# Optimization experiments

Hardware: AMD Instinct MI355X
Metric: run time of the kernel (lower is better)

The kernel has to match this reference:

```python
import jax, jax.numpy as jnp
import numpy as np

EPS = 1e-12  # F.normalize eps

def _l2norm(t):
    n = jnp.linalg.norm(t, axis=-1, keepdims=True)
    return t / jnp.maximum(n, EPS)

def setup_inputs() -> dict:
    key = jax.random.key(0)
    ks = jax.random.split(key, 6)
    B, S, H, M = 4, 4096, 1024, 256
    x = jax.random.normal(ks[0], (B, S, H), dtype=jnp.float32)
    W_query = jax.random.normal(ks[1], (M, H), dtype=jnp.float32) * 0.02
    W_key = jax.random.normal(ks[2], (M, H), dtype=jnp.float32) * 0.02
    W_value = jax.random.normal(ks[3], (M, H), dtype=jnp.float32) * 0.02
    W_out = jax.random.normal(ks[4], (H, M), dtype=jnp.float32) * 0.02
    M0 = jnp.zeros((M, M), dtype=jnp.float32)
    return {"x": x, "W_query": W_query, "W_key": W_key, "W_value": W_value,
            "W_out": W_out, "M0": M0, "chunk_size": 64}

def reference(x, W_query, W_key, W_value, W_out, M0, chunk_size):
    B, S, H = x.shape
    Mdim = W_query.shape[0]
    decay, max_m_norm = 0.99, 10.0
    q = jnp.einsum('bsh,mh->bsm', x, W_query)
    k = _l2norm(jnp.einsum('bsh,mh->bsm', x, W_key))
    v = _l2norm(jnp.einsum('bsh,mh->bsm', x, W_value))
    n_chunks = S // chunk_size
    c = chunk_size
    # (n_chunks, B, c, Mdim) so scan iterates over chunks
    qc = q.reshape(B, n_chunks, c, Mdim).transpose(1, 0, 2, 3)
    kc = k.reshape(B, n_chunks, c, Mdim).transpose(1, 0, 2, 3)
    vc = v.reshape(B, n_chunks, c, Mdim).transpose(1, 0, 2, 3)

    def step(Mst, qkv):
        qch, kch, vch = qkv
        # read with state at start of chunk: q @ M.T
        r = jnp.einsum('bcm,nm->bcn', qch, Mst)
        # uniform write, token-level aggregation
        outer = jnp.einsum('bci,bcj->ij', vch, kch) / (B * c)
        Mn = decay * Mst + outer
        nrm = jnp.linalg.norm(Mn)
        Mn = Mn * (max_m_norm / jnp.maximum(nrm, max_m_norm))
        return Mn, r

    _, r_all = jax.lax.scan(step, M0, (qc, kc, vc))  # (n_chunks, B, c, Mdim)
    retrieved = r_all.transpose(1, 0, 2, 3).reshape(B, S, Mdim)
    out = jnp.einsum('bsm,hm->bsh', retrieved, W_out)
    return out
```

## Files before the change

kernel.cpp:

```cpp
#include <hip/hip_runtime.h>
#include <hip/hip_bf16.h>


typedef __attribute__((ext_vector_type(4))) float  f4;
typedef __attribute__((ext_vector_type(8))) short  bf16x8;

constexpr int   Hdim  = 1024;
constexpr int   Md    = 256;
constexpr int   Ttok  = 16384;
constexpr float DECAY = 0.99f;
constexpr float MAXN  = 10.0f;

__device__ __forceinline__ unsigned short f2bf(float f) {
  union { float f; unsigned u; } v; v.f = f;
  unsigned r = v.u + 0x7FFFu + ((v.u >> 16) & 1u);
  return (unsigned short)(r >> 16);
}
__device__ __forceinline__ float bf2f(unsigned short h) {
  union { unsigned u; float f; } v; v.u = ((unsigned)h) << 16; return v.f;
}
__device__ __forceinline__ unsigned pk2bf(float a, float b) {
  __hip_bfloat162 h = __float22bfloat162_rn(make_float2(a, b));
  unsigned u; __builtin_memcpy(&u, &h, 4); return u;
}

__global__ __launch_bounds__(256) void k1_proj(
    const float* __restrict__ x, const float* __restrict__ Wq,
    const float* __restrict__ Wk, const float* __restrict__ Wv,
    unsigned short* __restrict__ qp, unsigned short* __restrict__ kb,
    unsigned short* __restrict__ vb)
{
  __shared__ unsigned short Als[128][40];
  __shared__ unsigned short Bls[128][40];
  const int tid  = threadIdx.x;
  const int g    = blockIdx.x;
  const int xcd  = g & 7, wq_ = g >> 3;
  const int ntile = wq_ % 6;
  const int strip = xcd * 16 + wq_ / 6;
  const int row0 = strip * 128;
  const int n0   = ntile * 128;
  const int seg  = n0 >> 8;
  const int nw0  = n0 & 255;
  const float* Wseg = (seg == 0) ? Wq : ((seg == 1) ? Wk : Wv);
  unsigned short* dst = (seg == 0) ? qp : ((seg == 1) ? kb : vb);

  const int tk = tid & 7, tr = tid >> 3;
  const int lane = tid & 63, wid = tid >> 6;
  const int wm = wid & 1, wn = wid >> 1;
  const int lr = lane & 15, lq = lane >> 4;

  f4 acc[4][4];
#pragma unroll
  for (int i = 0; i < 4; ++i)
#pragma unroll
    for (int j = 0; j < 4; ++j) acc[i][j] = f4{0.f, 0.f, 0.f, 0.f};

  for (int kk = 0; kk < Hdim; kk += 32) {
#pragma unroll
    for (int p = 0; p < 4; ++p) {
      int row = tr + 32 * p;
      float4 av = *(const float4*)&x[(long)(row0 + row) * Hdim + kk + tk * 4];
      *(uint2*)&Als[row][tk * 4] = make_uint2(pk2bf(av.x, av.y), pk2bf(av.z, av.w));
      float4 bv = *(const float4*)&Wseg[(long)(nw0 + row) * Hdim + kk + tk * 4];
      *(uint2*)&Bls[row][tk * 4] = make_uint2(pk2bf(bv.x, bv.y), pk2bf(bv.z, bv.w));
    }
    __syncthreads();
    bf16x8 af[4], bfr[4];
#pragma unroll
    for (int i = 0; i < 4; ++i) af[i]  = *(const bf16x8*)&Als[wm * 64 + i * 16 + lr][lq * 8];
#pragma unroll
    for (int j = 0; j < 4; ++j) bfr[j] = *(const bf16x8*)&Bls[wn * 64 + j * 16 + lr][lq * 8];
#pragma unroll
    for (int i = 0; i < 4; ++i)
#pragma unroll
      for (int j = 0; j < 4; ++j)
        acc[i][j] = __builtin_amdgcn_mfma_f32_16x16x32_bf16(af[i], bfr[j], acc[i][j], 0, 0, 0);
    __syncthreads();
  }
#pragma unroll
  for (int i = 0; i < 4; ++i)
#pragma unroll
    for (int rr = 0; rr < 4; ++rr) {
      int token = row0 + wm * 64 + i * 16 + lq * 4 + rr;
      int b = token >> 12, s = token & 4095;
      int pidx = (s >> 6) * 256 + b * 64 + (s & 63);
#pragma unroll
      for (int j = 0; j < 4; ++j) {
        int nn = nw0 + wn * 64 + j * 16 + lr;
        dst[pidx * Md + nn] = f2bf(acc[i][j][rr]);
      }
    }
}

__global__ __launch_bounds__(256) void k2_norms(
    const unsigned short* __restrict__ kb, const unsigned short* __restrict__ vb,
    float* __restrict__ innk, float* __restrict__ innv, float* __restrict__ D)
{
  const int tid = threadIdx.x;
  if (blockIdx.x == 0)
    for (int i = tid; i < 4096; i += 256) D[i] = 0.f;
  const int wid = tid >> 6, lane = tid & 63;
  const int row = blockIdx.x * 4 + wid;
  const unsigned short* p = (row < Ttok) ? (kb + (long)row * Md) : (vb + (long)(row - Ttok) * Md);
  ushort4 v = *(const ushort4*)&p[lane * 4];
  float f0 = bf2f(v.x), f1 = bf2f(v.y), f2 = bf2f(v.z), f3 = bf2f(v.w);
  float s = f0 * f0 + f1 * f1 + f2 * f2 + f3 * f3;
#pragma unroll
  for (int off = 32; off; off >>= 1) s += __shfl_xor(s, off);
  if (lane == 0) {
    float inv = 1.0f / fmaxf(sqrtf(s), 1e-12f);
    if (row < Ttok) innk[row] = inv; else innv[row - Ttok] = inv;
  }
}

__global__ __launch_bounds__(256) void k3_outer(
    const unsigned short* __restrict__ kb, const unsigned short* __restrict__ vb,
    const float* __restrict__ innk, const float* __restrict__ innv,
    float* __restrict__ O)
{
  __shared__ unsigned short Als[64][40];
  __shared__ unsigned short Bls[256][40];
  const int tid = threadIdx.x;
  const int t  = blockIdx.y;
  const int i0 = blockIdx.x * 64;
  const int lane = tid & 63, wid = tid >> 6;
  const int lr = lane & 15, lq = lane >> 4;

  f4 acc[16];
#pragma unroll
  for (int q = 0; q < 16; ++q) acc[q] = f4{0.f, 0.f, 0.f, 0.f};

  for (int tok0 = 0; tok0 < 256; tok0 += 32) {
    {
      int il = tid & 63, tl0 = tid >> 6;
#pragma unroll
      for (int p = 0; p < 8; ++p) {
        int tl = tl0 + 4 * p;
        int pidx = t * 256 + tok0 + tl;
        float sc = innv[pidx];
        Als[il][tl] = f2bf(bf2f(vb[(long)pidx * Md + i0 + il]) * sc);
      }
    }
    {
      int j4 = (tid & 63) * 4, tl0 = tid >> 6;
#pragma unroll
      for (int p = 0; p < 8; ++p) {
        int tl = tl0 + 4 * p;
        int pidx = t * 256 + tok0 + tl;
        float sc = innk[pidx];
        ushort4 kv = *(const ushort4*)&kb[(long)pidx * Md + j4];
        Bls[j4 + 0][tl] = f2bf(bf2f(kv.x) * sc);
        Bls[j4 + 1][tl] = f2bf(bf2f(kv.y) * sc);
        Bls[j4 + 2][tl] = f2bf(bf2f(kv.z) * sc);
        Bls[j4 + 3][tl] = f2bf(bf2f(kv.w) * sc);
      }
    }
    __syncthreads();
    bf16x8 af = *(const bf16x8*)&Als[wid * 16 + lr][lq * 8];
#pragma unroll
    for (int j = 0; j < 16; ++j) {
      bf16x8 bfr = *(const bf16x8*)&Bls[j * 16 + lr][lq * 8];
      acc[j] = __builtin_amdgcn_mfma_f32_16x16x32_bf16(af, bfr, acc[j], 0, 0, 0);
    }
    __syncthreads();
  }
  float* Ot = O + (long)t * 65536;
#pragma unroll
  for (int j = 0; j < 16; ++j)
#pragma unroll
    for (int rr = 0; rr < 4; ++rr) {
      int i = i0 + wid * 16 + lq * 4 + rr;
      Ot[i * 256 + j * 16 + lr] = acc[j][rr] * (1.0f / 256.0f);
    }
}

__global__ __launch_bounds__(256) void k4_gram(const float* __restrict__ O, float* __restrict__ D)
{
  __shared__ unsigned short Tls[64][40];
  const int tid = threadIdx.x;
  const int kbase = blockIdx.x * 256;
  const int lane = tid & 63, wid = tid >> 6;
  const int lr = lane & 15, lq = lane >> 4;
  f4 acc[4];
#pragma unroll
  for (int q = 0; q < 4; ++q) acc[q] = f4{0.f, 0.f, 0.f, 0.f};

  for (int kk = 0; kk < 256; kk += 32) {
    int tk = tid & 7, tr = tid >> 3;
#pragma unroll
    for (int p = 0; p < 2; ++p) {
      int row = tr + 32 * p;
      float4 v = *(const float4*)&O[(long)row * 65536 + kbase + kk + tk * 4];
      *(uint2*)&Tls[row][tk * 4] = make_uint2(pk2bf(v.x, v.y), pk2bf(v.z, v.w));
    }
    __syncthreads();
    bf16x8 af = *(const bf16x8*)&Tls[wid * 16 + lr][lq * 8];
#pragma unroll
    for (int nt = 0; nt < 4; ++nt) {
      bf16x8 bfr = *(const bf16x8*)&Tls[nt * 16 + lr][lq * 8];
      acc[nt] = __builtin_amdgcn_mfma_f32_16x16x32_bf16(af, bfr, acc[nt], 0, 0, 0);
    }
    __syncthreads();
  }
#pragma unroll
  for (int nt = 0; nt < 4; ++nt)
#pragma unroll
    for (int rr = 0; rr < 4; ++rr)
      atomicAdd(&D[(wid * 16 + lq * 4 + rr) * 64 + nt * 16 + lr], acc[nt][rr]);
}

__global__ __launch_bounds__(256) void k56_mstate(const float* __restrict__ O,
    const float* __restrict__ D, unsigned short* __restrict__ Mb)
{
  __shared__ float Dl[64 * 65];
  __shared__ float sarr[64];
  const int tid = threadIdx.x;
  const int col = blockIdx.x * 256 + tid;
  float ov[64];
#pragma unroll
  for (int j = 0; j < 64; ++j) ov[j] = O[(long)j * 65536 + col];
  for (int i = tid; i < 4096; i += 256) Dl[(i >> 6) * 65 + (i & 63)] = D[i];
  __syncthreads();
  if (tid < 64) {
    const int lane = tid;
    float w = 0.f, nm2 = 0.f;
    for (int t = 0; t < 64; ++t) {
      float wt   = __shfl(w, t);
      float Dtt  = Dl[t * 65 + t];
      float nmn2 = DECAY * DECAY * nm2 + 2.f * DECAY * wt + Dtt;
      float nrm  = sqrtf(fmaxf(nmn2, 0.f));
      float s    = MAXN / fmaxf(nrm, MAXN);
      if (lane == 0) sarr[t] = s;
      w   = s * (DECAY * w + Dl[t * 65 + lane]);
      nm2 = s * s * nmn2;
    }
  }
  __syncthreads();
  float m = 0.f;
#pragma unroll
  for (int t = 0; t < 64; ++t) {
    Mb[(long)t * 65536 + col] = f2bf(m);
    m = sarr[t] * (DECAY * m + ov[t]);
  }
}

__global__ __launch_bounds__(256) void k7_rgemm(
    const unsigned short* __restrict__ qp, const unsigned short* __restrict__ Mb,
    unsigned short* __restrict__ rb)
{
  __shared__ unsigned short Als[128][40];
  __shared__ unsigned short Bls[128][40];
  const int tid = threadIdx.x;
  const int t = blockIdx.z;
  const int row0 = t * 256 + blockIdx.y * 128;
  const int n0 = blockIdx.x * 128;
  const int lane = tid & 63, wid = tid >> 6;
  const int wm = wid & 1, wn = wid >> 1;
  const int lr = lane & 15, lq = lane >> 4;

  f4 acc[4][4];
#pragma unroll
  for (int i = 0; i < 4; ++i)
#pragma unroll
    for (int j = 0; j < 4; ++j) acc[i][j] = f4{0.f, 0.f, 0.f, 0.f};

  for (int kk = 0; kk < 256; kk += 32) {
    int kcol = (tid & 3) * 8, row = tid >> 2;
#pragma unroll
    for (int p = 0; p < 2; ++p) {
      *(bf16x8*)&Als[row + 64 * p][kcol] =
          *(const bf16x8*)&qp[(long)(row0 + row + 64 * p) * Md + kk + kcol];
      *(bf16x8*)&Bls[row + 64 * p][kcol] =
          *(const bf16x8*)&Mb[(long)t * 65536 + (n0 + row + 64 * p) * Md + kk + kcol];
    }
    __syncthreads();
    bf16x8 af[4], bfr[4];
#pragma unroll
    for (int i = 0; i < 4; ++i) af[i]  = *(const bf16x8*)&Als[wm * 64 + i * 16 + lr][lq * 8];
#pragma unroll
    for (int j = 0; j < 4; ++j) bfr[j] = *(const bf16x8*)&Bls[wn * 64 + j * 16 + lr][lq * 8];
#pragma unroll
    for (int i = 0; i < 4; ++i)
#pragma unroll
      for (int j = 0; j < 4; ++j)
        acc[i][j] = __builtin_amdgcn_mfma_f32_16x16x32_bf16(af[i], bfr[j], acc[i][j], 0, 0, 0);
    __syncthreads();
  }
#pragma unroll
  for (int i = 0; i < 4; ++i)
#pragma unroll
    for (int rr = 0; rr < 4; ++rr) {
      int prow = row0 + wm * 64 + i * 16 + lq * 4 + rr;
#pragma unroll
      for (int j = 0; j < 4; ++j) {
        int n = n0 + wn * 64 + j * 16 + lr;
        rb[(long)prow * Md + n] = f2bf(acc[i][j][rr]);
      }
    }
}

__global__ __launch_bounds__(256) void k8_out(
    const unsigned short* __restrict__ rb, const float* __restrict__ Wo,
    float* __restrict__ out)
{
  __shared__ unsigned short Als[128][40];
  __shared__ unsigned short Bls[128][40];
  const int tid = threadIdx.x;
  const int g = blockIdx.x;
  const int xcd = g & 7, wq_ = g >> 3;
  const int ntile = wq_ & 7;
  const int strip = xcd * 16 + (wq_ >> 3);
  const int n0 = ntile * 128;
  const int row0 = strip * 128;
  const int lane = tid & 63, wid = tid >> 6;
  const int wm = wid & 1, wn = wid >> 1;
  const int lr = lane & 15, lq = lane >> 4;

  f4 acc[4][4];
#pragma unroll
  for (int i = 0; i < 4; ++i)
#pragma unroll
    for (int j = 0; j < 4; ++j) acc[i][j] = f4{0.f, 0.f, 0.f, 0.f};

  for (int kk = 0; kk < 256; kk += 32) {
    {
      int kcol = (tid & 3) * 8, row = tid >> 2;
#pragma unroll
      for (int p = 0; p < 2; ++p)
        *(bf16x8*)&Als[row + 64 * p][kcol] =
            *(const bf16x8*)&rb[(long)(row0 + row + 64 * p) * Md + kk + kcol];
    }
    {
      int tk = tid & 7, tr = tid >> 3;
#pragma unroll
      for (int p = 0; p < 4; ++p) {
        int row = tr + 32 * p;
        float4 v = *(const float4*)&Wo[(long)(n0 + row) * Md + kk + tk * 4];
        *(uint2*)&Bls[row][tk * 4] = make_uint2(pk2bf(v.x, v.y), pk2bf(v.z, v.w));
      }
    }
    __syncthreads();
    bf16x8 af[4], bfr[4];
#pragma unroll
    for (int i = 0; i < 4; ++i) af[i]  = *(const bf16x8*)&Als[wm * 64 + i * 16 + lr][lq * 8];
#pragma unroll
    for (int j = 0; j < 4; ++j) bfr[j] = *(const bf16x8*)&Bls[wn * 64 + j * 16 + lr][lq * 8];
#pragma unroll
    for (int i = 0; i < 4; ++i)
#pragma unroll
      for (int j = 0; j < 4; ++j)
        acc[i][j] = __builtin_amdgcn_mfma_f32_16x16x32_bf16(af[i], bfr[j], acc[i][j], 0, 0, 0);
    __syncthreads();
  }
#pragma unroll
  for (int i = 0; i < 4; ++i)
#pragma unroll
    for (int rr = 0; rr < 4; ++rr) {
      int pidx = row0 + wm * 64 + i * 16 + lq * 4 + rr;
      int t = pidx >> 8, rm = pidx & 255;
      int token = (rm >> 6) * 4096 + t * 64 + (rm & 63);
#pragma unroll
      for (int j = 0; j < 4; ++j) {
        int h = n0 + wn * 64 + j * 16 + lr;
        out[(long)token * Hdim + h] = acc[i][j][rr];
      }
    }
}

extern "C" void kernel_launch(void* const* d_in, const int* in_sizes, int n_in,
                              void* d_out, int out_size, void* d_ws, size_t ws_size,
                              hipStream_t stream) {
  (void)in_sizes; (void)n_in; (void)out_size; (void)ws_size;
  const float* x  = (const float*)d_in[0];
  const float* Wq = (const float*)d_in[1];
  const float* Wk = (const float*)d_in[2];
  const float* Wv = (const float*)d_in[3];
  const float* Wo = (const float*)d_in[4];
  float* out = (float*)d_out;
  char* ws = (char*)d_ws;

  unsigned short* qp = (unsigned short*)(ws + 0);
  unsigned short* kb = (unsigned short*)(ws + 8388608);
  unsigned short* vb = (unsigned short*)(ws + 16777216);
  float* O    = (float*)(ws + 25165824);
  float* D    = (float*)(ws + 41943040);
  float* innk = (float*)(ws + 41959424);
  float* innv = (float*)(ws + 42024960);
  unsigned short* Mb = vb;
  unsigned short* rb = kb;

  k1_proj  <<<768,            256, 0, stream>>>(x, Wq, Wk, Wv, qp, kb, vb);
  k2_norms <<<8192,           256, 0, stream>>>(kb, vb, innk, innv, D);
  k3_outer <<<dim3(4, 64),    256, 0, stream>>>(kb, vb, innk, innv, O);
  k4_gram  <<<256,            256, 0, stream>>>(O, D);
  k56_mstate<<<256,           256, 0, stream>>>(O, D, Mb);
  k7_rgemm <<<dim3(2, 2, 64), 256, 0, stream>>>(qp, Mb, rb);
  k8_out   <<<1024,           256, 0, stream>>>(rb, Wo, out);
}
```

Before: 257.0 us.

## Pre-convert weights to bf16 and stage GEMM tiles via direct global-to-LDS loads

Adds a small kernel that converts Wq/Wk/Wv/Wo to bf16 once per call, so the projection and output GEMMs read half-size weights with no per-tile conversion. The three GEMM kernels now use global_load_lds 16-byte direct copies into XOR-swizzled LDS tiles with a K step of 64. k1 keeps x in fp32 in LDS and converts it to bf16 while building MFMA fragments. k3 also vectorizes its V loads. This trades an extra launch and larger LDS tiles (fp32 A tile in k1) for fewer register round-trips, fewer bank conflicts and fewer barriers per K.

```diff
diff --git a/kernel.cpp b/kernel.cpp
--- a/kernel.cpp
+++ b/kernel.cpp
@@ -23,31 +23,52 @@
   __hip_bfloat162 h = __float22bfloat162_rn(make_float2(a, b));
   unsigned u; __builtin_memcpy(&u, &h, 4); return u;
 }
+__device__ __forceinline__ void gll16(const void* gptr, void* lptr) {
+  __builtin_amdgcn_global_load_lds(
+      (const __attribute__((address_space(1))) unsigned int*)gptr,
+      (__attribute__((address_space(3))) unsigned int*)lptr, 16, 0, 0);
+}
+
+__global__ __launch_bounds__(256) void k0_wcvt(
+    const float* __restrict__ Wq, const float* __restrict__ Wk,
+    const float* __restrict__ Wv, const float* __restrict__ Wo,
+    unsigned short* __restrict__ Wb, unsigned short* __restrict__ Wob)
+{
+  int gid = blockIdx.x * 256 + threadIdx.x;
+  const float* src; unsigned short* dst; int off;
+  if (gid < 32768)      { src = Wq; dst = Wb;          off = gid; }
+  else if (gid < 65536) { src = Wk; dst = Wb + 262144; off = gid - 32768; }
+  else if (gid < 98304) { src = Wv; dst = Wb + 524288; off = gid - 65536; }
+  else                  { src = Wo; dst = Wob;         off = gid - 98304; }
+  float4 a = ((const float4*)src)[off * 2];
+  float4 b = ((const float4*)src)[off * 2 + 1];
+  ((uint4*)dst)[off] = make_uint4(pk2bf(a.x, a.y), pk2bf(a.z, a.w),
+                                  pk2bf(b.x, b.y), pk2bf(b.z, b.w));
+}
 
 __global__ __launch_bounds__(256) void k1_proj(
-    const float* __restrict__ x, const float* __restrict__ Wq,
-    const float* __restrict__ Wk, const float* __restrict__ Wv,
+    const float* __restrict__ x, const unsigned short* __restrict__ Wb,
     unsigned short* __restrict__ qp, unsigned short* __restrict__ kb,
     unsigned short* __restrict__ vb)
 {
-  __shared__ unsigned short Als[128][40];
-  __shared__ unsigned short Bls[128][40];
-  const int tid  = threadIdx.x;
-  const int g    = blockIdx.x;
-  const int xcd  = g & 7, wq_ = g >> 3;
+  __shared__ float          As[128 * 64];
+  __shared__ unsigned short Bs[128 * 64];
+  const int tid = threadIdx.x;
+  const int g = blockIdx.x;
+  const int xcd = g & 7, wq_ = g >> 3;
   const int ntile = wq_ % 6;
   const int strip = xcd * 16 + wq_ / 6;
   const int row0 = strip * 128;
-  const int n0   = ntile * 128;
-  const int seg  = n0 >> 8;
-  const int nw0  = n0 & 255;
-  const float* Wseg = (seg == 0) ? Wq : ((seg == 1) ? Wk : Wv);
+  const int n0 = ntile * 128;
+  const int seg = n0 >> 8;
+  const int nw0 = n0 & 255;
   unsigned short* dst = (seg == 0) ? qp : ((seg == 1) ? kb : vb);
 
-  const int tk = tid & 7, tr = tid >> 3;
   const int lane = tid & 63, wid = tid >> 6;
   const int wm = wid & 1, wn = wid >> 1;
   const int lr = lane & 15, lq = lane >> 4;
+  const int arow_l = lane >> 4, aseg_l = lane & 15;
+  const int brow_l = lane >> 3, bseg_l = lane & 7;
 
   f4 acc[4][4];
 #pragma unroll
@@ -55,26 +76,47 @@
 #pragma unroll
     for (int j = 0; j < 4; ++j) acc[i][j] = f4{0.f, 0.f, 0.f, 0.f};
 
-  for (int kk = 0; kk < Hdim; kk += 32) {
-#pragma unroll
-    for (int p = 0; p < 4; ++p) {
-      int row = tr + 32 * p;
-      float4 av = *(const float4*)&x[(long)(row0 + row) * Hdim + kk + tk * 4];
-      *(uint2*)&Als[row][tk * 4] = make_uint2(pk2bf(av.x, av.y), pk2bf(av.z, av.w));
-      float4 bv = *(const float4*)&Wseg[(long)(nw0 + row) * Hdim + kk + tk * 4];
-      *(uint2*)&Bls[row][tk * 4] = make_uint2(pk2bf(bv.x, bv.y), pk2bf(bv.z, bv.w));
-    }
-    __syncthreads();
-    bf16x8 af[4], bfr[4];
-#pragma unroll
-    for (int i = 0; i < 4; ++i) af[i]  = *(const bf16x8*)&Als[wm * 64 + i * 16 + lr][lq * 8];
-#pragma unroll
-    for (int j = 0; j < 4; ++j) bfr[j] = *(const bf16x8*)&Bls[wn * 64 + j * 16 + lr][lq * 8];
-#pragma unroll
-    for (int i = 0; i < 4; ++i)
-#pragma unroll
-      for (int j = 0; j < 4; ++j)
-        acc[i][j] = __builtin_amdgcn_mfma_f32_16x16x32_bf16(af[i], bfr[j], acc[i][j], 0, 0, 0);
+  for (int kk = 0; kk < Hdim; kk += 64) {
+#pragma unroll
+    for (int i = 0; i < 8; ++i) {
+      int r = wid * 32 + i * 4 + arow_l;
+      int s = aseg_l ^ (r & 15);
+      gll16(&x[(long)(row0 + r) * Hdim + kk + s * 4], &As[(wid * 32 + i * 4) * 64]);
+    }
+#pragma unroll
+    for (int i = 0; i < 4; ++i) {
+      int r = wid * 32 + i * 8 + brow_l;
+      int s = bseg_l ^ (r & 7);
+      gll16(&Wb[(long)(n0 + r) * Hdim + kk + s * 8], &Bs[(wid * 32 + i * 8) * 64]);
+    }
+    __syncthreads();
+#pragma unroll
+    for (int ks = 0; ks < 2; ++ks) {
+      bf16x8 af[4], bfr[4];
+#pragma unroll
+      for (int i = 0; i < 4; ++i) {
+        int m = wm * 64 + i * 16 + lr;
+        int p0 = (ks * 8 + lq * 2) ^ (m & 15);
+        int p1 = p0 ^ 1;
+        f4 a0 = *(const f4*)&As[m * 64 + p0 * 4];
+        f4 a1 = *(const f4*)&As[m * 64 + p1 * 4];
+        union { bf16x8 v; unsigned u[4]; } au;
+        au.u[0] = pk2bf(a0[0], a0[1]); au.u[1] = pk2bf(a0[2], a0[3]);
+        au.u[2] = pk2bf(a1[0], a1[1]); au.u[3] = pk2bf(a1[2], a1[3]);
+        af[i] = au.v;
+      }
+#pragma unroll
+      for (int j = 0; j < 4; ++j) {
+        int n = wn * 64 + j * 16 + lr;
+        int pb = (ks * 4 + lq) ^ (n & 7);
+        bfr[j] = *(const bf16x8*)&Bs[n * 64 + pb * 8];
+      }
+#pragma unroll
+      for (int i = 0; i < 4; ++i)
+#pragma unroll
+        for (int j = 0; j < 4; ++j)
+          acc[i][j] = __builtin_amdgcn_mfma_f32_16x16x32_bf16(af[i], bfr[j], acc[i][j], 0, 0, 0);
+    }
     __syncthreads();
   }
 #pragma unroll
@@ -87,7 +129,7 @@
 #pragma unroll
       for (int j = 0; j < 4; ++j) {
         int nn = nw0 + wn * 64 + j * 16 + lr;
-        dst[pidx * Md + nn] = f2bf(acc[i][j][rr]);
+        dst[(long)pidx * Md + nn] = f2bf(acc[i][j][rr]);
       }
     }
 }
@@ -132,13 +174,17 @@
 
   for (int tok0 = 0; tok0 < 256; tok0 += 32) {
     {
-      int il = tid & 63, tl0 = tid >> 6;
-#pragma unroll
-      for (int p = 0; p < 8; ++p) {
-        int tl = tl0 + 4 * p;
+      int i4 = (tid & 15) * 4, tl0 = tid >> 4;
+#pragma unroll
+      for (int p = 0; p < 2; ++p) {
+        int tl = tl0 + 16 * p;
         int pidx = t * 256 + tok0 + tl;
         float sc = innv[pidx];
-        Als[il][tl] = f2bf(bf2f(vb[(long)pidx * Md + i0 + il]) * sc);
+        ushort4 vv = *(const ushort4*)&vb[(long)pidx * Md + i0 + i4];
+        Als[i4 + 0][tl] = f2bf(bf2f(vv.x) * sc);
+        Als[i4 + 1][tl] = f2bf(bf2f(vv.y) * sc);
+        Als[i4 + 2][tl] = f2bf(bf2f(vv.z) * sc);
+        Als[i4 + 3][tl] = f2bf(bf2f(vv.w) * sc);
       }
     }
     {
@@ -248,15 +294,17 @@
     const unsigned short* __restrict__ qp, const unsigned short* __restrict__ Mb,
     unsigned short* __restrict__ rb)
 {
-  __shared__ unsigned short Als[128][40];
-  __shared__ unsigned short Bls[128][40];
+  __shared__ unsigned short As[128 * 64];
+  __shared__ unsigned short Bs[128 * 64];
   const int tid = threadIdx.x;
   const int t = blockIdx.z;
   const int row0 = t * 256 + blockIdx.y * 128;
   const int n0 = blockIdx.x * 128;
+  const unsigned short* Bsrc = Mb + (long)t * 65536;
   const int lane = tid & 63, wid = tid >> 6;
   const int wm = wid & 1, wn = wid >> 1;
   const int lr = lane & 15, lq = lane >> 4;
+  const int brow_l = lane >> 3, bseg_l = lane & 7;
 
   f4 acc[4][4];
 #pragma unroll
@@ -264,26 +312,36 @@
 #pragma unroll
     for (int j = 0; j < 4; ++j) acc[i][j] = f4{0.f, 0.f, 0.f, 0.f};
 
-  for (int kk = 0; kk < 256; kk += 32) {
-    int kcol = (tid & 3) * 8, row = tid >> 2;
-#pragma unroll
-    for (int p = 0; p < 2; ++p) {
-      *(bf16x8*)&Als[row + 64 * p][kcol] =
-          *(const bf16x8*)&qp[(long)(row0 + row + 64 * p) * Md + kk + kcol];
-      *(bf16x8*)&Bls[row + 64 * p][kcol] =
-          *(const bf16x8*)&Mb[(long)t * 65536 + (n0 + row + 64 * p) * Md + kk + kcol];
-    }
-    __syncthreads();
-    bf16x8 af[4], bfr[4];
-#pragma unroll
-    for (int i = 0; i < 4; ++i) af[i]  = *(const bf16x8*)&Als[wm * 64 + i * 16 + lr][lq * 8];
-#pragma unroll
-    for (int j = 0; j < 4; ++j) bfr[j] = *(const bf16x8*)&Bls[wn * 64 + j * 16 + lr][lq * 8];
-#pragma unroll
-    for (int i = 0; i < 4; ++i)
-#pragma unroll
-      for (int j = 0; j < 4; ++j)
-        acc[i][j] = __builtin_amdgcn_mfma_f32_16x16x32_bf16(af[i], bfr[j], acc[i][j], 0, 0, 0);
+  for (int kk = 0; kk < Md; kk += 64) {
+#pragma unroll
+    for (int i = 0; i < 4; ++i) {
+      int r = wid * 32 + i * 8 + brow_l;
+      int s = bseg_l ^ (r & 7);
+      gll16(&qp[(long)(row0 + r) * Md + kk + s * 8], &As[(wid * 32 + i * 8) * 64]);
+      gll16(&Bsrc[(long)(n0 + r) * Md + kk + s * 8], &Bs[(wid * 32 + i * 8) * 64]);
+    }
+    __syncthreads();
+#pragma unroll
+    for (int ks = 0; ks < 2; ++ks) {
+      bf16x8 af[4], bfr[4];
+#pragma unroll
+      for (int i = 0; i < 4; ++i) {
+        int m = wm * 64 + i * 16 + lr;
+        int pa = (ks * 4 + lq) ^ (m & 7);
+        af[i] = *(const bf16x8*)&As[m * 64 + pa * 8];
+      }
+#pragma unroll
+      for (int j = 0; j < 4; ++j) {
+        int n = wn * 64 + j * 16 + lr;
+        int pb = (ks * 4 + lq) ^ (n & 7);
+        bfr[j] = *(const bf16x8*)&Bs[n * 64 + pb * 8];
+      }
+#pragma unroll
+      for (int i = 0; i < 4; ++i)
+#pragma unroll
+        for (int j = 0; j < 4; ++j)
+          acc[i][j] = __builtin_amdgcn_mfma_f32_16x16x32_bf16(af[i], bfr[j], acc[i][j], 0, 0, 0);
+    }
     __syncthreads();
   }
 #pragma unroll
@@ -300,11 +358,11 @@
 }
 
 __global__ __launch_bounds__(256) void k8_out(
-    const unsigned short* __restrict__ rb, const float* __restrict__ Wo,
+    const unsigned short* __restrict__ rb, const unsigned short* __restrict__ Wob,
     float* __restrict__ out)
 {
-  __shared__ unsigned short Als[128][40];
-  __shared__ unsigned short Bls[128][40];
+  __shared__ unsigned short As[128 * 64];
+  __shared__ unsigned short Bs[128 * 64];
   const int tid = threadIdx.x;
   const int g = blockIdx.x;
   const int xcd = g & 7, wq_ = g >> 3;
@@ -315,6 +373,7 @@
   const int lane = tid & 63, wid = tid >> 6;
   const int wm = wid & 1, wn = wid >> 1;
   const int lr = lane & 15, lq = lane >> 4;
+  const int brow_l = lane >> 3, bseg_l = lane & 7;
 
   f4 acc[4][4];
 #pragma unroll
@@ -322,34 +381,36 @@
 #pragma unroll
     for (int j = 0; j < 4; ++j) acc[i][j] = f4{0.f, 0.f, 0.f, 0.f};
 
-  for (int kk = 0; kk < 256; kk += 32) {
-    {
-      int kcol = (tid & 3) * 8, row = tid >> 2;
-#pragma unroll
-      for (int p = 0; p < 2; ++p)
-        *(bf16x8*)&Als[row + 64 * p][kcol] =
-            *(const bf16x8*)&rb[(long)(row0 + row + 64 * p) * Md + kk + kcol];
-    }
-    {
-      int tk = tid & 7, tr = tid >> 3;
-#pragma unroll
-      for (int p = 0; p < 4; ++p) {
-        int row = tr + 32 * p;
-        float4 v = *(const float4*)&Wo[(long)(n0 + row) * Md + kk + tk * 4];
-        *(uint2*)&Bls[row][tk * 4] = make_uint2(pk2bf(v.x, v.y), pk2bf(v.z, v.w));
-      }
-    }
-    __syncthreads();
-    bf16x8 af[4], bfr[4];
-#pragma unroll
-    for (int i = 0; i < 4; ++i) af[i]  = *(const bf16x8*)&Als[wm * 64 + i * 16 + lr][lq * 8];
-#pragma unroll
-    for (int j = 0; j < 4; ++j) bfr[j] = *(const bf16x8*)&Bls[wn * 64 + j * 16 + lr][lq * 8];
-#pragma unroll
-    for (int i = 0; i < 4; ++i)
-#pragma unroll
-      for (int j = 0; j < 4; ++j)
-        acc[i][j] = __builtin_amdgcn_mfma_f32_16x16x32_bf16(af[i], bfr[j], acc[i][j], 0, 0, 0);
+  for (int kk = 0; kk < Md; kk += 64) {
+#pragma unroll
+    for (int i = 0; i < 4; ++i) {
+      int r = wid * 32 + i * 8 + brow_l;
+      int s = bseg_l ^ (r & 7);
+      gll16(&rb[(long)(row0 + r) * Md + kk + s * 8], &As[(wid * 32 + i * 8) * 64]);
+      gll16(&Wob[(long)(n0 + r) * Md + kk + s * 8], &Bs[(wid * 32 + i * 8) * 64]);
+    }
+    __syncthreads();
+#pragma unroll
+    for (int ks = 0; ks < 2; ++ks) {
+      bf16x8 af[4], bfr[4];
+#pragma unroll
+      for (int i = 0; i < 4; ++i) {
+        int m = wm * 64 + i * 16 + lr;
+        int pa = (ks * 4 + lq) ^ (m & 7);
+        af[i] = *(const bf16x8*)&As[m * 64 + pa * 8];
+      }
+#pragma unroll
+      for (int j = 0; j < 4; ++j) {
+        int n = wn * 64 + j * 16 + lr;
+        int pb = (ks * 4 + lq) ^ (n & 7);
+        bfr[j] = *(const bf16x8*)&Bs[n * 64 + pb * 8];
+      }
+#pragma unroll
+      for (int i = 0; i < 4; ++i)
+#pragma unroll
+        for (int j = 0; j < 4; ++j)
+          acc[i][j] = __builtin_amdgcn_mfma_f32_16x16x32_bf16(af[i], bfr[j], acc[i][j], 0, 0, 0);
+    }
     __syncthreads();
   }
 #pragma unroll
@@ -379,21 +440,24 @@
   float* out = (float*)d_out;
   char* ws = (char*)d_ws;
 
-  unsigned short* qp = (unsigned short*)(ws + 0);
-  unsigned short* kb = (unsigned short*)(ws + 8388608);
-  unsigned short* vb = (unsigned short*)(ws + 16777216);
+  unsigned short* qp  = (unsigned short*)(ws + 0);
+  unsigned short* kb  = (unsigned short*)(ws + 8388608);
+  unsigned short* vb  = (unsigned short*)(ws + 16777216);
   float* O    = (float*)(ws + 25165824);
   float* D    = (float*)(ws + 41943040);
   float* innk = (float*)(ws + 41959424);
   float* innv = (float*)(ws + 42024960);
+  unsigned short* Wb  = (unsigned short*)(ws + 42090496);
+  unsigned short* Wob = (unsigned short*)(ws + 43663360);
   unsigned short* Mb = vb;
   unsigned short* rb = kb;
 
-  k1_proj  <<<768,            256, 0, stream>>>(x, Wq, Wk, Wv, qp, kb, vb);
+  k0_wcvt  <<<512,            256, 0, stream>>>(Wq, Wk, Wv, Wo, Wb, Wob);
+  k1_proj  <<<768,            256, 0, stream>>>(x, Wb, qp, kb, vb);
   k2_norms <<<8192,           256, 0, stream>>>(kb, vb, innk, innv, D);
   k3_outer <<<dim3(4, 64),    256, 0, stream>>>(kb, vb, innk, innv, O);
   k4_gram  <<<256,            256, 0, stream>>>(O, D);
   k56_mstate<<<256,           256, 0, stream>>>(O, D, Mb);
   k7_rgemm <<<dim3(2, 2, 64), 256, 0, stream>>>(qp, Mb, rb);
-  k8_out   <<<1024,           256, 0, stream>>>(rb, Wo, out);
-}
+  k8_out   <<<1024,           256, 0, stream>>>(rb, Wob, out);
+}
```

After: 251.4 us. 1.02x faster.
